# Optimization experiments

Hardware: AMD Instinct MI355X
Metric: run time of the kernel (lower is better)

## Reference

```python
import jax, jax.numpy as jnp
import numpy as np

B, T, V, D, DH, H = 4, 512, 32000, 768, 768, 4  # batch, seq, vocab, dim_in, dim_out(per-head & ffn), heads


def layer_norm(x, g, b, eps=1e-5):
    m = jnp.mean(x, axis=-1, keepdims=True)
    v = jnp.mean((x - m) ** 2, axis=-1, keepdims=True)
    return (x - m) * jax.lax.rsqrt(v + eps) * g + b


def setup_inputs() -> dict:
    key = jax.random.key(0)
    ks = jax.random.split(key, 20)
    s = 0.02
    f = lambda k, shp: (jax.random.normal(k, shp, jnp.float32) * s)
    return {
        "x": jax.random.randint(ks[0], (B, T), 0, V),
        "attention_mask": jax.random.randint(ks[1], (B, 1, T), 0, 2).astype(bool),
        "token_embed": f(ks[2], (V, D)),
        "segment_embed": f(ks[3], (V, D)),
        "ln_embed_g": jnp.ones((D,), jnp.float32), "ln_embed_b": jnp.zeros((D,), jnp.float32),
        "Wq": f(ks[4], (H, D, DH)), "bq": f(ks[5], (H, DH)),
        "Wk": f(ks[6], (H, D, DH)), "bk": f(ks[7], (H, DH)),
        "Wv": f(ks[8], (H, D, DH)), "bv": f(ks[9], (H, DH)),
        "Wo": f(ks[10], (H * DH, D)), "bo": f(ks[11], (D,)),
        "ln_attn_g": jnp.ones((D,), jnp.float32), "ln_attn_b": jnp.zeros((D,), jnp.float32),
        "W1": f(ks[12], (D, DH)), "b1": f(ks[13], (DH,)),
        "W2": f(ks[14], (DH, D)), "b2": f(ks[15], (D,)),
        "ln_enc_g": jnp.ones((D,), jnp.float32), "ln_enc_b": jnp.zeros((D,), jnp.float32),
        "Wproj": f(ks[16], (D, V)), "bproj": f(ks[17], (V,)),
        "Wcls": f(ks[18], (D, 2)), "bcls": f(ks[19], (2,)),
    }


def reference(x, attention_mask, token_embed, segment_embed, ln_embed_g, ln_embed_b,
              Wq, bq, Wk, bk, Wv, bv, Wo, bo, ln_attn_g, ln_attn_b,
              W1, b1, W2, b2, ln_enc_g, ln_enc_b, Wproj, bproj, Wcls, bcls):
    Bsz, Tlen = x.shape
    dim = token_embed.shape[1]
    # JointEmbedding: segment tensor is 0 for first half, 1 afterwards
    seg = jnp.zeros_like(x).at[:, Tlen // 2 + 1:].set(1)
    # positional encoding (faithful to source: exponent is 2*j/dim per column j,
    # sin on even columns, cos on odd columns, applied to pos/10000**exp)
    d = 2.0 * jnp.arange(dim, dtype=jnp.float32) / dim            # [D]
    p = jnp.arange(Tlen, dtype=jnp.float32)[:, None] / (10000.0 ** d)  # [T, D]
    pe = jnp.where(jnp.arange(dim) % 2 == 0, jnp.sin(p), jnp.cos(p))   # [T, D]
    emb = token_embed[x] + segment_embed[seg] + pe[None]          # [B, T, D]
    emb = layer_norm(emb, ln_embed_g, ln_embed_b)

    # Multi-head attention (vectorized over the per-head Python loop)
    Q = jnp.einsum('btd,hde->bhte', emb, Wq) + bq[None, :, None, :]
    K = jnp.einsum('btd,hde->bhte', emb, Wk) + bk[None, :, None, :]
    Vh = jnp.einsum('btd,hde->bhte', emb, Wv) + bv[None, :, None, :]
    # NOTE: source scales by seq_len**-0.5 (Q.size(1)), not head_dim**-0.5
    scores = jnp.einsum('bhte,bhse->bhts', Q, K) * (float(Tlen) ** -0.5)
    # NOTE: source masked_fill_'s with value 1e-9 (not -inf) before softmax
    scores = jnp.where(attention_mask[:, None, :, :], 1e-9, scores)
    attn = jax.nn.softmax(scores, axis=-1)
    ctx = jnp.einsum('bhts,bhse->bhte', attn, Vh)                 # [B, H, T, DH]
    cat = ctx.transpose(0, 2, 1, 3).reshape(Bsz, Tlen, -1)        # head concat order
    attn_out = layer_norm(cat @ Wo + bo, ln_attn_g, ln_attn_b)

    # FFN (no residual in source; dropout is identity at inference)
    h = jax.nn.gelu(attn_out @ W1 + b1, approximate=False)
    enc = layer_norm(h @ W2 + b2, ln_enc_g, ln_enc_b)

    token_pred = enc @ Wproj + bproj                              # [B, T, V]
    logits = jax.nn.log_softmax(token_pred, axis=-1)
    cls_out = enc[:, 0, :] @ Wcls + bcls                          # [B, 2]
    return logits, cls_out
```

## Files before the change

### kernel.cpp

```cpp
#include <hip/hip_runtime.h>
#include <hip/hip_bf16.h>
#include <stdint.h>

#define B_ 4
#define T_ 512
#define V_ 32000
#define D_ 768
#define DH_ 768
#define H_ 4
#define R_ 2048

typedef unsigned short u16;
typedef __attribute__((ext_vector_type(4))) float f32x4;
typedef __attribute__((ext_vector_type(8))) short s16x8;
typedef __attribute__((address_space(3))) char* lds_cp;
typedef const __attribute__((address_space(1))) char* gl_cp;

__device__ __forceinline__ float bf2f(u16 u){
  union { float f; unsigned int i; } w; w.i = ((unsigned int)u) << 16; return w.f;
}
__device__ __forceinline__ u16 f2bf(float f){
  union { float f; unsigned int i; } w; w.f = f;
  unsigned int r = w.i + 0x7fffu + ((w.i >> 16) & 1u);
  return (u16)(r >> 16);
}

__device__ __forceinline__ float block_sum(float v, float* red){
  #pragma unroll
  for (int o = 32; o; o >>= 1) v += __shfl_down(v, o);
  __syncthreads();
  if ((threadIdx.x & 63) == 0) red[threadIdx.x >> 6] = v;
  __syncthreads();
  return red[0] + red[1] + red[2] + red[3];
}
__device__ __forceinline__ float block_max(float v, float* red){
  #pragma unroll
  for (int o = 32; o; o >>= 1) v = fmaxf(v, __shfl_down(v, o));
  __syncthreads();
  if ((threadIdx.x & 63) == 0) red[threadIdx.x >> 6] = v;
  __syncthreads();
  return fmaxf(fmaxf(red[0], red[1]), fmaxf(red[2], red[3]));
}

__global__ void mask_convert(const void* __restrict__ mraw, int* __restrict__ mout){
  __shared__ int isbyte;
  if (threadIdx.x == 0) isbyte = 0;
  __syncthreads();
  const unsigned char* by = (const unsigned char*)mraw;
  int f = 0;
  for (int i = threadIdx.x; i < 2048; i += 256)
    if ((i & 3) && by[i]) f = 1;
  if (f) atomicOr(&isbyte, 1);
  __syncthreads();
  if (isbyte){
    for (int i = threadIdx.x; i < 2048; i += 256) mout[i] = by[i] ? 1 : 0;
  } else {
    const int* mi = (const int*)mraw;
    for (int i = threadIdx.x; i < 2048; i += 256) mout[i] = mi[i] ? 1 : 0;
  }
}

__global__ __launch_bounds__(256)
void transpose_f2b(const float* __restrict__ in, u16* __restrict__ out, int R, int C){
  __shared__ u16 tile[32][33];
  long z = blockIdx.z;
  const float* inz = in + z * (long)R * C;
  u16* outz = out + z * (long)R * C;
  int c0 = blockIdx.x * 32, r0 = blockIdx.y * 32;
  int tx = threadIdx.x & 31, ty = threadIdx.x >> 5;
  #pragma unroll
  for (int i = 0; i < 32; i += 8)
    tile[ty + i][tx] = f2bf(inz[(long)(r0 + ty + i) * C + (c0 + tx)]);
  __syncthreads();
  #pragma unroll
  for (int i = 0; i < 32; i += 8)
    outz[(long)(c0 + ty + i) * R + (r0 + tx)] = tile[tx][ty + i];
}

__global__ __launch_bounds__(256)
void embed_ln(const int* __restrict__ x, const float* __restrict__ tok,
              const float* __restrict__ seg, const float* __restrict__ g,
              const float* __restrict__ bb, u16* __restrict__ emb){
  __shared__ float red[4];
  int r = blockIdx.x, t = r & 511;
  int tid = threadIdx.x;
  long trow = (long)x[r] * D_;
  long srow = (t > 256) ? (long)D_ : 0;
  float v[3];
  float s = 0.f;
  #pragma unroll
  for (int q = 0; q < 3; ++q){
    int j = tid + q * 256;
    float d = (2.0f * (float)j) * (1.0f / 768.0f);
    float p = (float)t * powf(10000.0f, -d);
    float pe = (j & 1) ? cosf(p) : sinf(p);
    v[q] = tok[trow + j] + seg[srow + j] + pe;
    s += v[q];
  }
  float mean = block_sum(s, red) * (1.0f / 768.0f);
  float vs = 0.f;
  #pragma unroll
  for (int q = 0; q < 3; ++q){ float dd = v[q] - mean; vs += dd * dd; }
  float var = block_sum(vs, red) * (1.0f / 768.0f);
  float inv = rsqrtf(var + 1e-5f);
  #pragma unroll
  for (int q = 0; q < 3; ++q){
    int j = tid + q * 256;
    emb[(long)r * D_ + j] = f2bf((v[q] - mean) * inv * g[j] + bb[j]);
  }
}

__global__ __launch_bounds__(256)
void ln_rows(const u16* __restrict__ in, const float* __restrict__ g,
             const float* __restrict__ bb, u16* __restrict__ out){
  __shared__ float red[4];
  long r = blockIdx.x;
  int tid = threadIdx.x;
  const u16* row = in + r * D_;
  float v[3];
  float s = 0.f;
  #pragma unroll
  for (int q = 0; q < 3; ++q){ v[q] = bf2f(row[tid + q * 256]); s += v[q]; }
  float mean = block_sum(s, red) * (1.0f / 768.0f);
  float vs = 0.f;
  #pragma unroll
  for (int q = 0; q < 3; ++q){ float dd = v[q] - mean; vs += dd * dd; }
  float var = block_sum(vs, red) * (1.0f / 768.0f);
  float inv = rsqrtf(var + 1e-5f);
  #pragma unroll
  for (int q = 0; q < 3; ++q){
    int j = tid + q * 256;
    out[r * D_ + j] = f2bf((v[q] - mean) * inv * g[j] + bb[j]);
  }
}

__global__ __launch_bounds__(256)
void attn_softmax(u16* __restrict__ S, const int* __restrict__ mask){
  __shared__ float red[4];
  int t = blockIdx.x, z = blockIdx.y, b = z >> 2;
  u16* row = S + (long)z * (T_ * T_) + (long)t * T_;
  int tid = threadIdx.x;
  int s0 = tid, s1 = tid + 256;
  float v0 = mask[b * T_ + s0] ? 1e-9f : bf2f(row[s0]);
  float v1 = mask[b * T_ + s1] ? 1e-9f : bf2f(row[s1]);
  float mx = block_max(fmaxf(v0, v1), red);
  float e0 = expf(v0 - mx), e1 = expf(v1 - mx);
  float l = block_sum(e0 + e1, red);
  float inv = 1.0f / l;
  row[s0] = f2bf(e0 * inv);
  row[s1] = f2bf(e1 * inv);
}

__global__ __launch_bounds__(256)
void log_softmax_rows(float* __restrict__ tp){
  __shared__ float sm[256], sl[256];
  long r = blockIdx.x;
  float* row = tp + r * (long)V_;
  f32x4* rv = (f32x4*)row;
  int tid = threadIdx.x;
  float m = -1e30f, l = 0.f;
  for (int c = tid; c < V_ / 4; c += 256){
    f32x4 v = rv[c];
    #pragma unroll
    for (int j = 0; j < 4; ++j){
      float x = v[j];
      if (x > m){ l = l * expf(m - x) + 1.0f; m = x; }
      else l += expf(x - m);
    }
  }
  sm[tid] = m; sl[tid] = l;
  __syncthreads();
  #pragma unroll
  for (int s = 128; s; s >>= 1){
    if (tid < s){
      float m2 = sm[tid + s], l2 = sl[tid + s];
      float M = fmaxf(sm[tid], m2);
      sl[tid] = sl[tid] * expf(sm[tid] - M) + l2 * expf(m2 - M);
      sm[tid] = M;
    }
    __syncthreads();
  }
  float lse = sm[0] + logf(sl[0]);
  for (int c = tid; c < V_ / 4; c += 256){
    f32x4 v = rv[c];
    #pragma unroll
    for (int j = 0; j < 4; ++j) v[j] -= lse;
    rv[c] = v;
  }
}

__global__ __launch_bounds__(256)
void cls_head(const u16* __restrict__ enc, const float* __restrict__ Wc,
              const float* __restrict__ bc, float* __restrict__ out){
  int w = threadIdx.x >> 6, lane = threadIdx.x & 63;
  const u16* e = enc + (long)w * (T_ * D_);
  float a0 = 0.f, a1 = 0.f;
  for (int k = lane; k < D_; k += 64){
    float ev = bf2f(e[k]);
    a0 += ev * Wc[k * 2 + 0];
    a1 += ev * Wc[k * 2 + 1];
  }
  #pragma unroll
  for (int o = 32; o; o >>= 1){ a0 += __shfl_down(a0, o); a1 += __shfl_down(a1, o); }
  if (lane == 0){
    out[(long)B_ * T_ * V_ + w * 2 + 0] = a0 + bc[0];
    out[(long)B_ * T_ * V_ + w * 2 + 1] = a1 + bc[1];
  }
}

template<int GELU, int F32OUT>
__global__ __launch_bounds__(256, 2)
void gemm_bt(const u16* __restrict__ A, const u16* __restrict__ Bt,
             const float* __restrict__ bias, void* __restrict__ Cv,
             int lda, int ldb,
             long sAzb, long sAzh, long sBzb, long sBzh, long sbz,
             long sCzb, long sCzh, long sCb, long sCr, long sCc,
             int zsh, float scale, int nt){
  extern __shared__ char smem[];
  u16* sA = (u16*)smem;
  u16* sB = sA + 2 * 128 * 64;
  int tid = threadIdx.x, lane = tid & 63, wid = tid >> 6;
  int wm = wid >> 1, wn = wid & 1;
  int lrow = lane & 15, lquad = lane >> 4;
  int z = blockIdx.z, zb = z >> zsh, zh = z & ((1 << zsh) - 1);
  long bm = (long)blockIdx.x * 128, bn = (long)blockIdx.y * 128;
  const u16* Az = A + zb * sAzb + zh * sAzh;
  const u16* Bz = Bt + zb * sBzb + zh * sBzh;

  f32x4 acc[4][4] = {};

  auto stage = [&](int buf, int kt){
    #pragma unroll
    for (int q = 0; q < 4; ++q){
      int seg = wid * 4 + q;
      int idx = seg * 64 + lane;
      int r = idx >> 3, c = idx & 7;
      int ksw = (c ^ (r & 7)) << 3;
      const u16* srcA = Az + (bm + r) * lda + kt * 64 + ksw;
      const u16* srcB = Bz + (bn + r) * ldb + kt * 64 + ksw;
      __builtin_amdgcn_global_load_lds((gl_cp)srcA,
          (lds_cp)((char*)(sA + buf * 8192) + seg * 1024), 16, 0, 0);
      __builtin_amdgcn_global_load_lds((gl_cp)srcB,
          (lds_cp)((char*)(sB + buf * 8192) + seg * 1024), 16, 0, 0);
    }
  };

  stage(0, 0);
  __syncthreads();
  int cur = 0;
  for (int t = 0; t < nt; ++t){
    if (t + 1 < nt) stage(cur ^ 1, t + 1);
    const u16* a0 = sA + cur * 8192;
    const u16* b0 = sB + cur * 8192;
    #pragma unroll
    for (int kk = 0; kk < 2; ++kk){
      int koff = (((kk * 4 + lquad) ^ (lrow & 7)) << 3);
      s16x8 af[4], bfv[4];
      #pragma unroll
      for (int m = 0; m < 4; ++m)
        af[m] = *(const s16x8*)(a0 + (wm * 64 + m * 16 + lrow) * 64 + koff);
      #pragma unroll
      for (int n = 0; n < 4; ++n)
        bfv[n] = *(const s16x8*)(b0 + (wn * 64 + n * 16 + lrow) * 64 + koff);
      #pragma unroll
      for (int m = 0; m < 4; ++m)
        #pragma unroll
        for (int n = 0; n < 4; ++n)
          acc[m][n] = __builtin_amdgcn_mfma_f32_16x16x32_bf16(af[m], bfv[n], acc[m][n], 0, 0, 0);
    }
    __syncthreads();
    cur ^= 1;
  }

  long czbase = zb * sCzb + zh * sCzh;
  #pragma unroll
  for (int n = 0; n < 4; ++n){
    long col = bn + wn * 64 + n * 16 + lrow;
    float bv = bias ? bias[zb * sbz + col] : 0.f;
    #pragma unroll
    for (int m = 0; m < 4; ++m){
      #pragma unroll
      for (int j = 0; j < 4; ++j){
        long row = bm + wm * 64 + m * 16 + lquad * 4 + j;
        float v = acc[m][n][j] * scale + bv;
        if (GELU) v = 0.5f * v * (1.0f + erff(v * 0.70710678118654752f));
        long ci = czbase + (row >> 9) * sCb + (row & 511) * sCr + col * sCc;
        if (F32OUT) ((float*)Cv)[ci] = v;
        else        ((u16*)Cv)[ci] = f2bf(v);
      }
    }
  }
}

extern "C" void kernel_launch(void* const* d_in, const int* in_sizes, int n_in,
                              void* d_out, int out_size, void* d_ws, size_t ws_size,
                              hipStream_t stream){
  const int*   x     = (const int*)d_in[0];
  const void*  amask = d_in[1];
  const float* tok = (const float*)d_in[2];
  const float* seg = (const float*)d_in[3];
  const float* lng = (const float*)d_in[4];
  const float* lnb = (const float*)d_in[5];
  const float* Wq  = (const float*)d_in[6];
  const float* bq  = (const float*)d_in[7];
  const float* Wk  = (const float*)d_in[8];
  const float* bk  = (const float*)d_in[9];
  const float* Wv  = (const float*)d_in[10];
  const float* bv  = (const float*)d_in[11];
  const float* Wo  = (const float*)d_in[12];
  const float* bo  = (const float*)d_in[13];
  const float* lag = (const float*)d_in[14];
  const float* lab = (const float*)d_in[15];
  const float* W1  = (const float*)d_in[16];
  const float* b1  = (const float*)d_in[17];
  const float* W2  = (const float*)d_in[18];
  const float* b2  = (const float*)d_in[19];
  const float* leg = (const float*)d_in[20];
  const float* leb = (const float*)d_in[21];
  const float* Wp  = (const float*)d_in[22];
  const float* bp  = (const float*)d_in[23];
  const float* Wc  = (const float*)d_in[24];
  const float* bc  = (const float*)d_in[25];
  float* out = (float*)d_out;
  char* ws = (char*)d_ws;

  size_t off = 0;
  auto alloc = [&](size_t bytes){ size_t o = off; off += (bytes + 255) & ~(size_t)255; return o; };
  size_t o_mask = alloc(2048 * 4);
  size_t o_emb  = alloc((size_t)R_ * D_ * 2);
  size_t o_wqT  = alloc((size_t)H_ * D_ * DH_ * 2);
  size_t o_wkT  = alloc((size_t)H_ * D_ * DH_ * 2);
  size_t o_wvT  = alloc((size_t)H_ * D_ * DH_ * 2);
  size_t o_woT  = alloc((size_t)3072 * 768 * 2);
  size_t o_w1T  = alloc((size_t)768 * 768 * 2);
  size_t o_w2T  = alloc((size_t)768 * 768 * 2);
  size_t o_Q    = alloc((size_t)B_ * H_ * T_ * DH_ * 2);
  size_t o_K    = alloc((size_t)B_ * H_ * T_ * DH_ * 2);
  size_t o_VT   = alloc((size_t)B_ * H_ * DH_ * T_ * 2);
  size_t o_S    = alloc((size_t)B_ * H_ * T_ * T_ * 2);
  size_t o_cat  = alloc((size_t)R_ * 3072 * 2);
  size_t o_ap   = alloc((size_t)R_ * D_ * 2);
  size_t o_ao   = alloc((size_t)R_ * D_ * 2);
  size_t o_h1   = alloc((size_t)R_ * D_ * 2);
  size_t o_ep   = alloc((size_t)R_ * D_ * 2);
  size_t o_enc  = alloc((size_t)R_ * D_ * 2);
  size_t o_wpT  = o_Q;
  if (ws_size < off) return;

  int* maskI = (int*)(ws + o_mask);
  u16* emb  = (u16*)(ws + o_emb);
  u16* wqT  = (u16*)(ws + o_wqT);
  u16* wkT  = (u16*)(ws + o_wkT);
  u16* wvT  = (u16*)(ws + o_wvT);
  u16* woT  = (u16*)(ws + o_woT);
  u16* w1T  = (u16*)(ws + o_w1T);
  u16* w2T  = (u16*)(ws + o_w2T);
  u16* Qb   = (u16*)(ws + o_Q);
  u16* Kb   = (u16*)(ws + o_K);
  u16* VTb  = (u16*)(ws + o_VT);
  u16* Sb   = (u16*)(ws + o_S);
  u16* catb = (u16*)(ws + o_cat);
  u16* apb  = (u16*)(ws + o_ap);
  u16* aob  = (u16*)(ws + o_ao);
  u16* h1b  = (u16*)(ws + o_h1);
  u16* epb  = (u16*)(ws + o_ep);
  u16* encb = (u16*)(ws + o_enc);
  u16* wpT  = (u16*)(ws + o_wpT);

  const long sQK_zb = (long)H_ * T_ * DH_;
  const long sQK_zh = (long)T_ * DH_;

  mask_convert<<<1, 256, 0, stream>>>(amask, maskI);
  transpose_f2b<<<dim3(24, 24, 4), 256, 0, stream>>>(Wq, wqT, 768, 768);
  transpose_f2b<<<dim3(24, 24, 4), 256, 0, stream>>>(Wk, wkT, 768, 768);
  transpose_f2b<<<dim3(24, 24, 4), 256, 0, stream>>>(Wv, wvT, 768, 768);
  transpose_f2b<<<dim3(24, 96, 1), 256, 0, stream>>>(Wo, woT, 3072, 768);
  transpose_f2b<<<dim3(24, 24, 1), 256, 0, stream>>>(W1, w1T, 768, 768);
  transpose_f2b<<<dim3(24, 24, 1), 256, 0, stream>>>(W2, w2T, 768, 768);
  embed_ln<<<R_, 256, 0, stream>>>(x, tok, seg, lng, lnb, emb);

  gemm_bt<0,0><<<dim3(16, 6, 4), 256, 65536, stream>>>(emb, wqT, bq, Qb,
      768, 768, 0, 0, (long)768 * 768, 0, 768,
      sQK_zh, 0, sQK_zb, 768, 1, 0, 1.0f, 12);
  gemm_bt<0,0><<<dim3(16, 6, 4), 256, 65536, stream>>>(emb, wkT, bk, Kb,
      768, 768, 0, 0, (long)768 * 768, 0, 768,
      sQK_zh, 0, sQK_zb, 768, 1, 0, 1.0f, 12);
  gemm_bt<0,0><<<dim3(16, 6, 4), 256, 65536, stream>>>(emb, wvT, bv, VTb,
      768, 768, 0, 0, (long)768 * 768, 0, 768,
      sQK_zh, 0, sQK_zb, 1, 512, 0, 1.0f, 12);

  gemm_bt<0,0><<<dim3(4, 4, 16), 256, 65536, stream>>>(Qb, Kb, nullptr, Sb,
      768, 768, sQK_zb, sQK_zh, sQK_zb, sQK_zh, 0,
      (long)H_ * T_ * T_, (long)T_ * T_, 0, 512, 1, 2, 0.044194173824159216f, 12);

  attn_softmax<<<dim3(512, 16), 256, 0, stream>>>(Sb, maskI);

  gemm_bt<0,0><<<dim3(4, 6, 16), 256, 65536, stream>>>(Sb, VTb, nullptr, catb,
      512, 512, (long)H_ * T_ * T_, (long)T_ * T_, sQK_zb, sQK_zh, 0,
      (long)T_ * 3072, 768, 0, 3072, 1, 2, 1.0f, 8);

  gemm_bt<0,0><<<dim3(16, 6, 1), 256, 65536, stream>>>(catb, woT, bo, apb,
      3072, 3072, 0, 0, 0, 0, 0,
      0, 0, (long)512 * 768, 768, 1, 0, 1.0f, 48);
  ln_rows<<<R_, 256, 0, stream>>>(apb, lag, lab, aob);

  gemm_bt<1,0><<<dim3(16, 6, 1), 256, 65536, stream>>>(aob, w1T, b1, h1b,
      768, 768, 0, 0, 0, 0, 0,
      0, 0, (long)512 * 768, 768, 1, 0, 1.0f, 12);
  gemm_bt<0,0><<<dim3(16, 6, 1), 256, 65536, stream>>>(h1b, w2T, b2, epb,
      768, 768, 0, 0, 0, 0, 0,
      0, 0, (long)512 * 768, 768, 1, 0, 1.0f, 12);
  ln_rows<<<R_, 256, 0, stream>>>(epb, leg, leb, encb);

  transpose_f2b<<<dim3(1000, 24, 1), 256, 0, stream>>>(Wp, wpT, 768, 32000);

  gemm_bt<0,1><<<dim3(16, 250, 1), 256, 65536, stream>>>(encb, wpT, bp, out,
      768, 768, 0, 0, 0, 0, 0,
      0, 0, (long)512 * V_, V_, 1, 0, 1.0f, 12);
  log_softmax_rows<<<R_, 256, 0, stream>>>(out);
  cls_head<<<1, 256, 0, stream>>>(encb, Wc, bc, out);

  (void)in_sizes; (void)n_in; (void)out_size;
}
```

Measured before the change: 559.9 us.

## Store vocab logits in bf16, remap GEMM workgroups per XCD, merge weight transposes

The vocab projection now writes bf16 logits to a workspace buffer, and a new log-softmax kernel reads them and writes fp32 output. This avoids writing and re-reading the large fp32 logits tensor twice. The GEMM remaps workgroup IDs so that consecutive tiles land on the same XCD, which is meant to improve L2 reuse. The six weight transposes are merged into one launch. The bf16 intermediate rounds the logits before log-softmax, which may cost some accuracy, and the bf16 path only runs when the workspace is large enough.

Measured after the change: 486.0 us. 13.2% less time.

```diff
diff --git a/kernel.cpp b/kernel.cpp
--- a/kernel.cpp
+++ b/kernel.cpp
@@ -13,6 +13,7 @@
 typedef unsigned short u16;
 typedef __attribute__((ext_vector_type(4))) float f32x4;
 typedef __attribute__((ext_vector_type(8))) short s16x8;
+typedef __attribute__((ext_vector_type(8))) unsigned short u16x8;
 typedef __attribute__((address_space(3))) char* lds_cp;
 typedef const __attribute__((address_space(1))) char* gl_cp;
 
@@ -61,20 +62,44 @@
 }
 
 __global__ __launch_bounds__(256)
+void transpose_all(const float* __restrict__ Wq, const float* __restrict__ Wk,
+                   const float* __restrict__ Wv, const float* __restrict__ Wo,
+                   const float* __restrict__ W1, const float* __restrict__ W2,
+                   u16* __restrict__ wqT, u16* __restrict__ wkT,
+                   u16* __restrict__ wvT, u16* __restrict__ woT,
+                   u16* __restrict__ w1T, u16* __restrict__ w2T){
+  __shared__ u16 tile[32][33];
+  int z = blockIdx.z;
+  const float* in; u16* out; int out_ld = 768;
+  if (z < 4)      { in = Wq + (long)z * 589824;        out = wqT + (long)z * 589824; }
+  else if (z < 8) { int k = z - 4;  in = Wk + (long)k * 589824; out = wkT + (long)k * 589824; }
+  else if (z < 12){ int k = z - 8;  in = Wv + (long)k * 589824; out = wvT + (long)k * 589824; }
+  else if (z < 16){ int k = z - 12; in = Wo + (long)k * 589824; out = woT + (long)k * 768; out_ld = 3072; }
+  else if (z == 16){ in = W1; out = w1T; }
+  else             { in = W2; out = w2T; }
+  int c0 = blockIdx.x * 32, r0 = blockIdx.y * 32;
+  int tx = threadIdx.x & 31, ty = threadIdx.x >> 5;
+  #pragma unroll
+  for (int i = 0; i < 32; i += 8)
+    tile[ty + i][tx] = f2bf(in[(long)(r0 + ty + i) * 768 + (c0 + tx)]);
+  __syncthreads();
+  #pragma unroll
+  for (int i = 0; i < 32; i += 8)
+    out[(long)(c0 + ty + i) * out_ld + (r0 + tx)] = tile[tx][ty + i];
+}
+
+__global__ __launch_bounds__(256)
 void transpose_f2b(const float* __restrict__ in, u16* __restrict__ out, int R, int C){
   __shared__ u16 tile[32][33];
-  long z = blockIdx.z;
-  const float* inz = in + z * (long)R * C;
-  u16* outz = out + z * (long)R * C;
   int c0 = blockIdx.x * 32, r0 = blockIdx.y * 32;
   int tx = threadIdx.x & 31, ty = threadIdx.x >> 5;
   #pragma unroll
   for (int i = 0; i < 32; i += 8)
-    tile[ty + i][tx] = f2bf(inz[(long)(r0 + ty + i) * C + (c0 + tx)]);
+    tile[ty + i][tx] = f2bf(in[(long)(r0 + ty + i) * C + (c0 + tx)]);
   __syncthreads();
   #pragma unroll
   for (int i = 0; i < 32; i += 8)
-    outz[(long)(c0 + ty + i) * R + (r0 + tx)] = tile[tx][ty + i];
+    out[(long)(c0 + ty + i) * R + (r0 + tx)] = tile[tx][ty + i];
 }
 
 __global__ __launch_bounds__(256)
@@ -152,6 +177,45 @@
 }
 
 __global__ __launch_bounds__(256)
+void lsm_b2f(const u16* __restrict__ pred, float* __restrict__ out){
+  __shared__ float sm[256], sl[256];
+  long r = blockIdx.x;
+  const u16x8* rv = (const u16x8*)(pred + r * (long)V_);
+  int tid = threadIdx.x;
+  float m = -1e30f, l = 0.f;
+  for (int c = tid; c < V_ / 8; c += 256){
+    u16x8 v = rv[c];
+    #pragma unroll
+    for (int j = 0; j < 8; ++j){
+      float x = bf2f(v[j]);
+      if (x > m){ l = l * expf(m - x) + 1.0f; m = x; }
+      else l += expf(x - m);
+    }
+  }
+  sm[tid] = m; sl[tid] = l;
+  __syncthreads();
+  #pragma unroll
+  for (int s = 128; s; s >>= 1){
+    if (tid < s){
+      float m2 = sm[tid + s], l2 = sl[tid + s];
+      float M = fmaxf(sm[tid], m2);
+      sl[tid] = sl[tid] * expf(sm[tid] - M) + l2 * expf(m2 - M);
+      sm[tid] = M;
+    }
+    __syncthreads();
+  }
+  float lse = sm[0] + logf(sl[0]);
+  f32x4* orow = (f32x4*)(out + r * (long)V_);
+  for (int c = tid; c < V_ / 8; c += 256){
+    u16x8 v = rv[c];
+    f32x4 o0, o1;
+    #pragma unroll
+    for (int j = 0; j < 4; ++j){ o0[j] = bf2f(v[j]) - lse; o1[j] = bf2f(v[j + 4]) - lse; }
+    orow[2 * c] = o0; orow[2 * c + 1] = o1;
+  }
+}
+
+__global__ __launch_bounds__(256)
 void log_softmax_rows(float* __restrict__ tp){
   __shared__ float sm[256], sl[256];
   long r = blockIdx.x;
@@ -222,8 +286,17 @@
   int tid = threadIdx.x, lane = tid & 63, wid = tid >> 6;
   int wm = wid >> 1, wn = wid & 1;
   int lrow = lane & 15, lquad = lane >> 4;
-  int z = blockIdx.z, zb = z >> zsh, zh = z & ((1 << zsh) - 1);
-  long bm = (long)blockIdx.x * 128, bn = (long)blockIdx.y * 128;
+
+  unsigned gx = gridDim.x, gy = gridDim.y;
+  unsigned nwg = gx * gy * gridDim.z;
+  unsigned id = blockIdx.x + gx * (blockIdx.y + gy * blockIdx.z);
+  unsigned qq = nwg >> 3, rr = nwg & 7, xcd = id & 7, loc = id >> 3;
+  unsigned nid = (xcd < rr ? xcd * (qq + 1) : rr * (qq + 1) + (xcd - rr) * qq) + loc;
+  unsigned bx = nid % gx, tmpq = nid / gx;
+  unsigned by = tmpq % gy, bz = tmpq / gy;
+
+  int z = (int)bz, zb = z >> zsh, zh = z & ((1 << zsh) - 1);
+  long bm = (long)bx * 128, bn = (long)by * 128;
   const u16* Az = A + zb * sAzb + zh * sAzh;
   const u16* Bz = Bt + zb * sBzb + zh * sBzh;
 
@@ -345,7 +418,10 @@
   size_t o_ep   = alloc((size_t)R_ * D_ * 2);
   size_t o_enc  = alloc((size_t)R_ * D_ * 2);
   size_t o_wpT  = o_Q;
-  if (ws_size < off) return;
+  size_t off_base = off;
+  size_t o_pred = alloc((size_t)R_ * V_ * 2);
+  int bigws = (ws_size >= off);
+  if (ws_size < off_base) return;
 
   int* maskI = (int*)(ws + o_mask);
   u16* emb  = (u16*)(ws + o_emb);
@@ -366,17 +442,14 @@
   u16* epb  = (u16*)(ws + o_ep);
   u16* encb = (u16*)(ws + o_enc);
   u16* wpT  = (u16*)(ws + o_wpT);
+  u16* predb = (u16*)(ws + o_pred);
 
   const long sQK_zb = (long)H_ * T_ * DH_;
   const long sQK_zh = (long)T_ * DH_;
 
   mask_convert<<<1, 256, 0, stream>>>(amask, maskI);
-  transpose_f2b<<<dim3(24, 24, 4), 256, 0, stream>>>(Wq, wqT, 768, 768);
-  transpose_f2b<<<dim3(24, 24, 4), 256, 0, stream>>>(Wk, wkT, 768, 768);
-  transpose_f2b<<<dim3(24, 24, 4), 256, 0, stream>>>(Wv, wvT, 768, 768);
-  transpose_f2b<<<dim3(24, 96, 1), 256, 0, stream>>>(Wo, woT, 3072, 768);
-  transpose_f2b<<<dim3(24, 24, 1), 256, 0, stream>>>(W1, w1T, 768, 768);
-  transpose_f2b<<<dim3(24, 24, 1), 256, 0, stream>>>(W2, w2T, 768, 768);
+  transpose_all<<<dim3(24, 24, 18), 256, 0, stream>>>(Wq, Wk, Wv, Wo, W1, W2,
+      wqT, wkT, wvT, woT, w1T, w2T);
   embed_ln<<<R_, 256, 0, stream>>>(x, tok, seg, lng, lnb, emb);
 
   gemm_bt<0,0><<<dim3(16, 6, 4), 256, 65536, stream>>>(emb, wqT, bq, Qb,
@@ -414,10 +487,17 @@
 
   transpose_f2b<<<dim3(1000, 24, 1), 256, 0, stream>>>(Wp, wpT, 768, 32000);
 
-  gemm_bt<0,1><<<dim3(16, 250, 1), 256, 65536, stream>>>(encb, wpT, bp, out,
-      768, 768, 0, 0, 0, 0, 0,
-      0, 0, (long)512 * V_, V_, 1, 0, 1.0f, 12);
-  log_softmax_rows<<<R_, 256, 0, stream>>>(out);
+  if (bigws){
+    gemm_bt<0,0><<<dim3(16, 250, 1), 256, 65536, stream>>>(encb, wpT, bp, predb,
+        768, 768, 0, 0, 0, 0, 0,
+        0, 0, (long)512 * V_, V_, 1, 0, 1.0f, 12);
+    lsm_b2f<<<R_, 256, 0, stream>>>(predb, out);
+  } else {
+    gemm_bt<0,1><<<dim3(16, 250, 1), 256, 65536, stream>>>(encb, wpT, bp, out,
+        768, 768, 0, 0, 0, 0, 0,
+        0, 0, (long)512 * V_, V_, 1, 0, 1.0f, 12);
+    log_softmax_rows<<<R_, 256, 0, stream>>>(out);
+  }
   cls_head<<<1, 256, 0, stream>>>(encb, Wc, bc, out);
 
   (void)in_sizes; (void)n_in; (void)out_size;
```
